# Optimization experiments

Measured on AMD Instinct MI355X. Metric: run time of the kernel, lower is better.

The kernel has to match this reference:

```python
import jax, jax.numpy as jnp
import numpy as np

C = 768           # input_embed_dim
G = 16            # conv groups
CG = C // G       # channels per group (48)
MAX_TOKENS = 64
N = 65536         # sequence / spatial length
B = 1             # .item() in the torch code forces batch == 1
EPS = 1e-5


def _layernorm(x, gamma, beta):
    mu = jnp.mean(x, axis=-1, keepdims=True)
    var = jnp.mean((x - mu) ** 2, axis=-1, keepdims=True)
    return (x - mu) * jax.lax.rsqrt(var + EPS) * gamma + beta


def _grouped_pointwise(x, w):
    # x: [B, N, C]; w: [G, CG_out, CG_in] (torch Conv2d weight [C, CG, 1, 1] regrouped)
    xg = x.reshape(x.shape[0], x.shape[1], G, CG)           # [B, N, G, CG]
    yg = jnp.einsum('bngi,goi->bngo', xg, w)                 # [B, N, G, CG]
    return yg.reshape(x.shape[0], x.shape[1], C)


def setup_inputs() -> dict:
    key = jax.random.key(0)
    ks = jax.random.split(key, 9)
    s = 1.0 / np.sqrt(CG)
    inp = {
        'x': jax.random.normal(ks[0], (B, N, C), dtype=jnp.float32),
        'tn_gamma': jnp.ones((C,), jnp.float32),
        'tn_beta': jnp.zeros((C,), jnp.float32),
        'w1': jax.random.uniform(ks[1], (G, CG, CG), jnp.float32, -s, s),   # grouped conv 1
        'w2': jax.random.uniform(ks[2], (MAX_TOKENS, C), jnp.float32, -1 / np.sqrt(C), 1 / np.sqrt(C)),  # pointwise conv C->MAX_TOKENS
        'wf': jax.random.uniform(ks[3], (G, CG, CG), jnp.float32, -s, s),   # grouped feat conv
        'pred_w': jax.random.uniform(ks[4], (C,), jnp.float32, -1 / np.sqrt(C), 1 / np.sqrt(C)),
        'pred_b': jax.random.uniform(ks[5], (1,), jnp.float32, -1 / np.sqrt(C), 1 / np.sqrt(C)),
        'n_gamma': jnp.ones((C,), jnp.float32),
        'n_beta': jnp.zeros((C,), jnp.float32),
    }
    return inp


def reference(x, tn_gamma, tn_beta, w1, w2, wf, pred_w, pred_b, n_gamma, n_beta):
    # LayerNorm over channels
    xn = _layernorm(x, tn_gamma, tn_beta)                    # [B, N, C]

    # token_predictor: AdaptiveAvgPool2d over (N,1) -> Linear(C,1) -> Sigmoid
    pooled = jnp.mean(xn, axis=1)                            # [B, C]
    ratio = jax.nn.sigmoid(pooled @ pred_w + pred_b[0])      # [B]
    # num_tokens = int(ratio.item() * MAX_TOKENS)  (truncation == floor, ratio > 0)
    num_tokens = jnp.floor(ratio[0] * MAX_TOKENS).astype(jnp.int32)
    tok_mask = (jnp.arange(MAX_TOKENS) < num_tokens)[None, :, None]  # [1, T, 1]

    # tokenLearner: grouped 1x1 conv -> ReLU -> pointwise conv C -> MAX_TOKENS
    h = jax.nn.relu(_grouped_pointwise(xn, w1))              # [B, N, C]
    scores = jnp.einsum('bnc,tc->btn', h, w2)                # [B, T, N]
    # softmax is per-token-row over N, so slicing rows before/after softmax is equivalent;
    # we mask dropped rows to zero (fixed output shape instead of dynamic slice).
    selected = jax.nn.softmax(scores, axis=-1)
    selected = jnp.where(tok_mask, selected, 0.0)            # [B, T, N]

    feat = _grouped_pointwise(xn, wf)                        # [B, N, C]
    out = jnp.einsum('btn,bnc->btc', selected, feat)         # [B, T, C]
    out = _layernorm(out, n_gamma, n_beta)
    out = jnp.where(tok_mask, out, 0.0)                      # zero rows beyond num_tokens
    return selected, out
```

## Files before the change

kernel.cpp:

```cpp
#include <hip/hip_runtime.h>
#include <hip/hip_bf16.h>

#define DEV __device__ __forceinline__

constexpr int N = 65536;
constexpr int C = 768;
constexpr int T = 64;

using bf16 = __hip_bfloat16;
using short8 = __attribute__((ext_vector_type(8))) short;
using f32x4  = __attribute__((ext_vector_type(4))) float;

DEV ushort f2bits(float v) { union { __hip_bfloat16 h; ushort u; } x; x.h = __float2bfloat16(v); return x.u; }
DEV float bits2f(ushort b) { union { uint u; float f; } x; x.u = ((uint)b) << 16; return x.f; }
DEV f32x4 mfma16(short8 a, short8 b, f32x4 c) { return __builtin_amdgcn_mfma_f32_16x16x32_bf16(a, b, c, 0, 0, 0); }
DEV int swz(int row, int col) { return row * 64 + (col ^ ((row & 7) << 3)); }

DEV float wredsum(float v) {
#pragma unroll
  for (int o = 32; o > 0; o >>= 1) v += __shfl_xor(v, o, 64);
  return v;
}

__global__ __launch_bounds__(256) void k_wprep(const float* __restrict__ w1,
                                               const float* __restrict__ w2,
                                               const float* __restrict__ wf,
                                               short* __restrict__ w1p,
                                               short* __restrict__ w2p,
                                               short* __restrict__ wfp) {
  const int b = blockIdx.x, tid = threadIdx.x;
  if (b < 192) {
    int idx = b * 256 + tid;
    int j = idx & 7, lane = (idx >> 3) & 63, u = idx >> 9;
    int kt = u & 1, v = u >> 1, ot = v % 3, g = v / 3;
    int o = ot * 16 + (lane & 15), k = kt * 32 + ((lane >> 4) & 3) * 8 + j;
    w1p[idx] = (k < 48) ? (short)f2bits(w1[g * 2304 + o * 48 + k]) : (short)0;
  } else if (b < 448) {
    int idx = (b - 192) * 256 + tid;
    int j = idx & 7, lane = (idx >> 3) & 63, u = idx >> 9;
    int kt = u & 1, v = u >> 1, tt = v & 3, g = v >> 2;
    int t = tt * 16 + (lane & 15), k = kt * 32 + ((lane >> 4) & 3) * 8 + j;
    w2p[idx] = (k < 48) ? (short)f2bits(w2[t * 768 + g * 48 + k]) : (short)0;
  } else {
    int idx = (b - 448) * 256 + tid;
    int j = idx & 7, lane = (idx >> 3) & 63, u = idx >> 9;
    int kt = u & 1, v = u >> 1, ot = v % 3, g = v / 3;
    int o = ot * 16 + (lane & 15), k = kt * 32 + ((lane >> 4) & 3) * 8 + j;
    wfp[idx] = (k < 48) ? (short)f2bits(wf[g * 2304 + o * 48 + k]) : (short)0;
  }
}

__global__ __launch_bounds__(256, 4) void k_ln(const float4* __restrict__ x,
                                               const float4* __restrict__ gam,
                                               const float4* __restrict__ bet,
                                               uint2* __restrict__ xn,
                                               float* __restrict__ pooled) {
  const int tid = threadIdx.x, wave = tid >> 6, lane = tid & 63;
  float4 gg[3], bb[3], pool[3];
#pragma unroll
  for (int j = 0; j < 3; j++) {
    gg[j] = gam[lane + 64 * j]; bb[j] = bet[lane + 64 * j];
    pool[j] = make_float4(0.f, 0.f, 0.f, 0.f);
  }
  const int r0 = (blockIdx.x * 4 + wave) * 16;
  for (int r = r0; r < r0 + 16; ++r) {
    const float4* xr = x + (size_t)r * 192;
    float4 v[3]; float s = 0.f, q = 0.f;
#pragma unroll
    for (int j = 0; j < 3; j++) {
      v[j] = xr[lane + 64 * j];
      s += v[j].x + v[j].y + v[j].z + v[j].w;
      q += v[j].x * v[j].x + v[j].y * v[j].y + v[j].z * v[j].z + v[j].w * v[j].w;
    }
    s = wredsum(s); q = wredsum(q);
    const float mu = s * (1.f / C);
    const float rs = rsqrtf(q * (1.f / C) - mu * mu + 1e-5f);
    uint2* xo = xn + (size_t)r * 192;
#pragma unroll
    for (int j = 0; j < 3; j++) {
      float y0 = (v[j].x - mu) * rs * gg[j].x + bb[j].x;
      float y1 = (v[j].y - mu) * rs * gg[j].y + bb[j].y;
      float y2 = (v[j].z - mu) * rs * gg[j].z + bb[j].z;
      float y3 = (v[j].w - mu) * rs * gg[j].w + bb[j].w;
      pool[j].x += y0; pool[j].y += y1; pool[j].z += y2; pool[j].w += y3;
      xo[lane + 64 * j] = make_uint2((uint)f2bits(y0) | ((uint)f2bits(y1) << 16),
                                     (uint)f2bits(y2) | ((uint)f2bits(y3) << 16));
    }
  }
  __shared__ float lp[4][C];
#pragma unroll
  for (int j = 0; j < 3; j++) {
    int base = (lane + 64 * j) * 4;
    lp[wave][base] = pool[j].x; lp[wave][base + 1] = pool[j].y;
    lp[wave][base + 2] = pool[j].z; lp[wave][base + 3] = pool[j].w;
  }
  __syncthreads();
  for (int c = tid; c < C; c += 256)
    atomicAdd(&pooled[c], lp[0][c] + lp[1][c] + lp[2][c] + lp[3][c]);
}

__global__ __launch_bounds__(256) void k_pool(const float* __restrict__ pooled,
                                              const float* __restrict__ pw,
                                              const float* __restrict__ pb,
                                              int* __restrict__ ntok) {
  const int tid = threadIdx.x, wave = tid >> 6, lane = tid & 63;
  float a = 0.f;
  for (int c = tid; c < C; c += 256) a += pooled[c] * (1.f / N) * pw[c];
  a = wredsum(a);
  __shared__ float red[4];
  if (lane == 0) red[wave] = a;
  __syncthreads();
  if (tid == 0) {
    float d = red[0] + red[1] + red[2] + red[3] + pb[0];
    float ratio = 1.f / (1.f + expf(-d));
    int nt = (int)floorf(ratio * 64.f);
    nt = nt < 0 ? 0 : (nt > 64 ? 64 : nt);
    *ntok = nt;
  }
}

__global__ __launch_bounds__(256, 4) void k_cs(const short* __restrict__ xn,
                                               const short* __restrict__ w1p,
                                               const short* __restrict__ w2p,
                                               float* __restrict__ scores) {
  __shared__ __align__(16) short hs[4][16 * 64];
  const int tid = threadIdx.x, wave = tid >> 6, lane = tid & 63;
  const int l15 = lane & 15, g2 = lane >> 4;
  short* hw = hs[wave];
  {
    uint* hz = (uint*)hw;
    for (int i = lane; i < 512; i += 64) hz[i] = 0u;
  }
  const int row0 = blockIdx.x * 64 + wave * 16;
  f32x4 acc[4];
#pragma unroll
  for (int t = 0; t < 4; ++t) acc[t] = (f32x4){0.f, 0.f, 0.f, 0.f};
  const short* xrow = xn + (size_t)(row0 + l15) * 768;
  const int lo8 = lane * 8;

  short8 bx0 = *(const short8*)(xrow + g2 * 8);
  short8 bx1 = *(const short8*)(xrow + 32 + g2 * 8);
  for (int g = 0; g < 16; ++g) {
    const int gn = (g < 15) ? g + 1 : 15;
    short8 nbx0 = *(const short8*)(xrow + gn * 48 + g2 * 8);
    short8 nbx1 = *(const short8*)(xrow + gn * 48 + 32 + g2 * 8);
    const short* w1g = w1p + g * 3072;
#pragma unroll
    for (int ot = 0; ot < 3; ++ot) {
      short8 a0 = *(const short8*)(w1g + (ot * 2 + 0) * 512 + lo8);
      short8 a1 = *(const short8*)(w1g + (ot * 2 + 1) * 512 + lo8);
      f32x4 h = (f32x4){0.f, 0.f, 0.f, 0.f};
      h = mfma16(a0, bx0, h);
      h = mfma16(a1, bx1, h);
      uint lo = (uint)f2bits(fmaxf(h[0], 0.f)) | ((uint)f2bits(fmaxf(h[1], 0.f)) << 16);
      uint hi = (uint)f2bits(fmaxf(h[2], 0.f)) | ((uint)f2bits(fmaxf(h[3], 0.f)) << 16);
      *(uint2*)&hw[swz(l15, ot * 16 + g2 * 4)] = make_uint2(lo, hi);
    }
    short8 hb0 = *(const short8*)&hw[swz(l15, g2 * 8)];
    short8 hb1 = *(const short8*)&hw[swz(l15, 32 + g2 * 8)];
    const short* w2g = w2p + g * 4096;
#pragma unroll
    for (int tt = 0; tt < 4; ++tt) {
      short8 a0 = *(const short8*)(w2g + (tt * 2 + 0) * 512 + lo8);
      short8 a1 = *(const short8*)(w2g + (tt * 2 + 1) * 512 + lo8);
      acc[tt] = mfma16(a0, hb0, acc[tt]);
      acc[tt] = mfma16(a1, hb1, acc[tt]);
    }
    bx0 = nbx0; bx1 = nbx1;
  }
#pragma unroll
  for (int tt = 0; tt < 4; ++tt)
#pragma unroll
    for (int r = 0; r < 4; ++r)
      scores[(size_t)(tt * 16 + g2 * 4 + r) * N + row0 + l15] = acc[tt][r];
}

__global__ __launch_bounds__(256) void k_stats(const float* __restrict__ scores,
                                               float2* __restrict__ part) {
  const int t = blockIdx.x >> 3, s = blockIdx.x & 7;
  const float* row = scores + (size_t)t * N + s * 8192;
  float m = -1e30f, l = 0.f;
  for (int i = threadIdx.x; i < 8192; i += 256) {
    float v = row[i];
    if (v > m) { l = l * __expf(m - v) + 1.f; m = v; }
    else       { l += __expf(v - m); }
  }
#pragma unroll
  for (int o = 32; o > 0; o >>= 1) {
    float m2 = __shfl_xor(m, o, 64), l2 = __shfl_xor(l, o, 64);
    float M = fmaxf(m, m2);
    l = l * __expf(m - M) + l2 * __expf(m2 - M); m = M;
  }
  __shared__ float sm[4], sl[4];
  const int wave = threadIdx.x >> 6, lane = threadIdx.x & 63;
  if (lane == 0) { sm[wave] = m; sl[wave] = l; }
  __syncthreads();
  if (threadIdx.x == 0) {
    float M = sm[0], L = sl[0];
    for (int w = 1; w < 4; w++) { float M2 = fmaxf(M, sm[w]); L = L * __expf(M - M2) + sl[w] * __expf(sm[w] - M2); M = M2; }
    part[blockIdx.x] = make_float2(M, L);
  }
}

__global__ void k_sfinal(const float2* __restrict__ part, float* __restrict__ Mv,
                         float* __restrict__ Li) {
  int t = threadIdx.x;
  float M = -1e30f, L = 0.f;
  for (int s = 0; s < 8; s++) {
    float2 p = part[t * 8 + s];
    float M2 = fmaxf(M, p.x);
    L = L * __expf(M - M2) + p.y * __expf(p.x - M2); M = M2;
  }
  Mv[t] = M; Li[t] = 1.f / L;
}

__global__ __launch_bounds__(256) void k_sel(const float* __restrict__ scores,
                                             const float* __restrict__ Mv,
                                             const float* __restrict__ Li,
                                             const int* __restrict__ ntokp,
                                             float* __restrict__ sel) {
  const int t = blockIdx.x >> 3, s = blockIdx.x & 7;
  const size_t base = (size_t)t * N + s * 8192;
  const bool on = t < *ntokp;
  const float m = Mv[t], li = Li[t];
  for (int i = threadIdx.x; i < 8192; i += 256)
    sel[base + i] = on ? __expf(scores[base + i] - m) * li : 0.f;
}

__global__ __launch_bounds__(512, 4) void k_og(const short* __restrict__ xn,
                                               const short* __restrict__ wfp,
                                               const float* __restrict__ sel,
                                               const int* __restrict__ ntokp,
                                               ushort* __restrict__ out_part) {
  __shared__ __align__(16) short ft[192 * 64];
  const int tid = threadIdx.x, wave = tid >> 6, lane = tid & 63;
  const int l15 = lane & 15, g2 = lane >> 4;
  const int cb = blockIdx.y, nb = blockIdx.x;
  const int ntok = *ntokp;
  const int tt = wave >> 1, chalf = wave & 1;
  const int gq = wave >> 1, ntq = wave & 1;
  const bool act = (tt * 16) < ntok;
  short8 wa0[3], wa1[3];
  {
    const short* wb = wfp + (size_t)(cb * 4 + gq) * 3072 + lane * 8;
#pragma unroll
    for (int ot = 0; ot < 3; ++ot) {
      wa0[ot] = *(const short8*)(wb + (ot * 2 + 0) * 512);
      wa1[ot] = *(const short8*)(wb + (ot * 2 + 1) * 512);
    }
  }
  f32x4 acc[6];
#pragma unroll
  for (int k = 0; k < 6; ++k) acc[k] = (f32x4){0.f, 0.f, 0.f, 0.f};

  for (int ns = 0; ns < 16; ++ns) {
    const int n0 = nb * 512 + ns * 32;
    __syncthreads();
    {
      const short* xr = xn + (size_t)(n0 + ntq * 16 + l15) * 768 + (cb * 4 + gq) * 48;
      short8 b0 = *(const short8*)(xr + g2 * 8);
      short8 b1 = *(const short8*)(xr + 32 + g2 * 8);
#pragma unroll
      for (int ot = 0; ot < 3; ++ot) {
        f32x4 d = (f32x4){0.f, 0.f, 0.f, 0.f};
        d = mfma16(wa0[ot], b0, d);
        d = mfma16(wa1[ot], b1, d);
        int n = ntq * 16 + l15;
#pragma unroll
        for (int r = 0; r < 4; ++r) {
          int c = gq * 48 + ot * 16 + g2 * 4 + r;
          ft[c * 64 + (n ^ ((c & 7) << 3))] = (short)f2bits(d[r]);
        }
      }
    }
    __syncthreads();
    if (act) {
      const float* sr = sel + (size_t)(tt * 16 + l15) * N + n0 + g2 * 8;
      float4 s0 = *(const float4*)sr;
      float4 s1 = *(const float4*)(sr + 4);
      short8 pa;
      pa[0] = (short)f2bits(s0.x); pa[1] = (short)f2bits(s0.y);
      pa[2] = (short)f2bits(s0.z); pa[3] = (short)f2bits(s0.w);
      pa[4] = (short)f2bits(s1.x); pa[5] = (short)f2bits(s1.y);
      pa[6] = (short)f2bits(s1.z); pa[7] = (short)f2bits(s1.w);
#pragma unroll
      for (int ct = 0; ct < 6; ++ct) {
        int c = (chalf * 6 + ct) * 16 + l15;
        short8 fb = *(const short8*)&ft[c * 64 + ((g2 * 8) ^ ((c & 7) << 3))];
        acc[ct] = mfma16(pa, fb, acc[ct]);
      }
    }
  }
#pragma unroll
  for (int ct = 0; ct < 6; ++ct)
#pragma unroll
    for (int r = 0; r < 4; ++r) {
      int t = tt * 16 + g2 * 4 + r;
      int c = cb * 192 + (chalf * 6 + ct) * 16 + l15;
      out_part[(size_t)nb * (64 * 768) + t * 768 + c] = f2bits(acc[ct][r]);
    }
}

__global__ __launch_bounds__(256) void k_red(const ushort* __restrict__ out_part,
                                             float* __restrict__ oacc) {
  int i = blockIdx.x * 256 + threadIdx.x;
  float s = 0.f;
  for (int nb = 0; nb < 128; ++nb) s += bits2f(out_part[(size_t)nb * (64 * 768) + i]);
  oacc[i] = s;
}

__global__ __launch_bounds__(256) void k_ofinal(const float* __restrict__ out_acc,
                                                const float* __restrict__ ng,
                                                const float* __restrict__ nb_,
                                                const int* __restrict__ ntokp,
                                                float* __restrict__ outp) {
  const int tid = threadIdx.x, wave = tid >> 6, lane = tid & 63;
  const int ntok = *ntokp;
  for (int t = wave; t < T; t += 4) {
    const float* r = out_acc + t * C;
    float v[12]; float s = 0.f;
#pragma unroll
    for (int j = 0; j < 12; j++) { v[j] = r[lane + 64 * j]; s += v[j]; }
    s = wredsum(s); float mu = s * (1.f / C);
    float q = 0.f;
#pragma unroll
    for (int j = 0; j < 12; j++) { float d = v[j] - mu; q += d * d; }
    q = wredsum(q); float rs = rsqrtf(q * (1.f / C) + 1e-5f);
    float* o = outp + t * C;
#pragma unroll
    for (int j = 0; j < 12; j++) {
      int c = lane + 64 * j;
      float y = (v[j] - mu) * rs * ng[c] + nb_[c];
      o[c] = (t < ntok) ? y : 0.f;
    }
  }
}

extern "C" void kernel_launch(void* const* d_in, const int* in_sizes, int n_in,
                              void* d_out, int out_size, void* d_ws, size_t ws_size,
                              hipStream_t stream) {
  const float* x  = (const float*)d_in[0];
  const float* tg = (const float*)d_in[1];
  const float* tb = (const float*)d_in[2];
  const float* w1 = (const float*)d_in[3];
  const float* w2 = (const float*)d_in[4];
  const float* wf = (const float*)d_in[5];
  const float* pw = (const float*)d_in[6];
  const float* pb = (const float*)d_in[7];
  const float* ng = (const float*)d_in[8];
  const float* nb = (const float*)d_in[9];

  char* ws = (char*)d_ws;
  float*  pooled = (float*)(ws + 0);
  float2* part   = (float2*)(ws + 4096);
  float*  Mv     = (float*)(ws + 8192);
  float*  Li     = (float*)(ws + 8448);
  int*    ntok   = (int*)(ws + 8704);
  short*  w1p    = (short*)(ws + 16384);
  short*  w2p    = (short*)(ws + 114688);
  short*  wfp    = (short*)(ws + 245760);
  short*  xn     = (short*)(ws + 344064);
  float*  scores = (float*)(ws + 101007360);
  ushort* opart  = (ushort*)(ws + 101007360);
  float*  oacc   = (float*)(ws + 113590272);

  float* sel  = (float*)d_out;
  float* outp = (float*)d_out + (size_t)T * N;

  hipMemsetAsync(pooled, 0, C * sizeof(float), stream);

  k_wprep <<<640, 256, 0, stream>>>(w1, w2, wf, w1p, w2p, wfp);
  k_ln    <<<1024, 256, 0, stream>>>((const float4*)x, (const float4*)tg, (const float4*)tb,
                                     (uint2*)xn, pooled);
  k_pool  <<<1, 256, 0, stream>>>(pooled, pw, pb, ntok);
  k_cs    <<<1024, 256, 0, stream>>>(xn, w1p, w2p, scores);
  k_stats <<<512, 256, 0, stream>>>(scores, part);
  k_sfinal<<<1, 64, 0, stream>>>(part, Mv, Li);
  k_sel   <<<512, 256, 0, stream>>>(scores, Mv, Li, ntok, sel);
  k_og    <<<dim3(128, 4), 512, 0, stream>>>(xn, wfp, sel, ntok, opart);
  k_red   <<<192, 256, 0, stream>>>(opart, oacc);
  k_ofinal<<<1, 256, 0, stream>>>(oacc, ng, nb, ntok, outp);
}
```

Measured before the change: 465.4 us.

## Double-buffer LDS in score and output kernels, fuse softmax finalisation and reductions

Several changes land together. k_cs gets a double-buffered per-wave h tile and a 2x unroll. k_sfinal is merged into k_sel, which now vectorises with float4 and also writes a bf16 copy of the selection matrix. k_og reads that bf16 copy instead of converting fp32, double-buffers its LDS feature tile with register prefetch of the next x and selection loads, cuts to one barrier per step, and packs LDS stores. k_red and k_ofinal are fused into one 64-block k_fin. The goal is fewer launches, less traffic and less barrier stalling, at the cost of extra LDS (which lowers k_og occupancy to 2), an extra bf16 write, and a one-pass variance that is less numerically robust.

Result: faster. 438.4 us (-5.8%).

```diff
diff --git a/kernel.cpp b/kernel.cpp
--- a/kernel.cpp
+++ b/kernel.cpp
@@ -123,13 +123,12 @@
                                                const short* __restrict__ w1p,
                                                const short* __restrict__ w2p,
                                                float* __restrict__ scores) {
-  __shared__ __align__(16) short hs[4][16 * 64];
+  __shared__ __align__(16) short hs[4][2][16 * 64];
   const int tid = threadIdx.x, wave = tid >> 6, lane = tid & 63;
   const int l15 = lane & 15, g2 = lane >> 4;
-  short* hw = hs[wave];
   {
-    uint* hz = (uint*)hw;
-    for (int i = lane; i < 512; i += 64) hz[i] = 0u;
+    uint* hz = (uint*)hs[wave];
+    for (int i = lane; i < 1024; i += 64) hz[i] = 0u;
   }
   const int row0 = blockIdx.x * 64 + wave * 16;
   f32x4 acc[4];
@@ -140,10 +139,12 @@
 
   short8 bx0 = *(const short8*)(xrow + g2 * 8);
   short8 bx1 = *(const short8*)(xrow + 32 + g2 * 8);
+#pragma unroll 2
   for (int g = 0; g < 16; ++g) {
     const int gn = (g < 15) ? g + 1 : 15;
     short8 nbx0 = *(const short8*)(xrow + gn * 48 + g2 * 8);
     short8 nbx1 = *(const short8*)(xrow + gn * 48 + 32 + g2 * 8);
+    short* hw = hs[wave][g & 1];
     const short* w1g = w1p + g * 3072;
 #pragma unroll
     for (int ot = 0; ot < 3; ++ot) {
@@ -202,94 +203,103 @@
   }
 }
 
-__global__ void k_sfinal(const float2* __restrict__ part, float* __restrict__ Mv,
-                         float* __restrict__ Li) {
-  int t = threadIdx.x;
+__global__ __launch_bounds__(256) void k_sel(const float* __restrict__ scores,
+                                             const float2* __restrict__ part,
+                                             const int* __restrict__ ntokp,
+                                             float* __restrict__ sel,
+                                             ushort* __restrict__ selb) {
+  const int t = blockIdx.x >> 3, s = blockIdx.x & 7;
   float M = -1e30f, L = 0.f;
-  for (int s = 0; s < 8; s++) {
-    float2 p = part[t * 8 + s];
+#pragma unroll
+  for (int i = 0; i < 8; i++) {
+    float2 p = part[t * 8 + i];
     float M2 = fmaxf(M, p.x);
     L = L * __expf(M - M2) + p.y * __expf(p.x - M2); M = M2;
   }
-  Mv[t] = M; Li[t] = 1.f / L;
-}
-
-__global__ __launch_bounds__(256) void k_sel(const float* __restrict__ scores,
-                                             const float* __restrict__ Mv,
-                                             const float* __restrict__ Li,
-                                             const int* __restrict__ ntokp,
-                                             float* __restrict__ sel) {
-  const int t = blockIdx.x >> 3, s = blockIdx.x & 7;
+  const float li = 1.f / L;
+  const bool on = t < *ntokp;
   const size_t base = (size_t)t * N + s * 8192;
-  const bool on = t < *ntokp;
-  const float m = Mv[t], li = Li[t];
-  for (int i = threadIdx.x; i < 8192; i += 256)
-    sel[base + i] = on ? __expf(scores[base + i] - m) * li : 0.f;
-}
-
-__global__ __launch_bounds__(512, 4) void k_og(const short* __restrict__ xn,
+  const float4* sp = (const float4*)(scores + base);
+  float4* op = (float4*)(sel + base);
+  uint2* ob = (uint2*)(selb + base);
+#pragma unroll
+  for (int it = 0; it < 8; ++it) {
+    int idx = threadIdx.x + 256 * it;
+    float4 v = sp[idx];
+    float4 e;
+    e.x = on ? __expf(v.x - M) * li : 0.f;
+    e.y = on ? __expf(v.y - M) * li : 0.f;
+    e.z = on ? __expf(v.z - M) * li : 0.f;
+    e.w = on ? __expf(v.w - M) * li : 0.f;
+    op[idx] = e;
+    ob[idx] = make_uint2((uint)f2bits(e.x) | ((uint)f2bits(e.y) << 16),
+                         (uint)f2bits(e.z) | ((uint)f2bits(e.w) << 16));
+  }
+}
+
+__global__ __launch_bounds__(512, 2) void k_og(const short* __restrict__ xn,
                                                const short* __restrict__ wfp,
-                                               const float* __restrict__ sel,
+                                               const short* __restrict__ selb,
                                                const int* __restrict__ ntokp,
                                                ushort* __restrict__ out_part) {
-  __shared__ __align__(16) short ft[192 * 64];
+  __shared__ __align__(16) short ft[2][192 * 64];
   const int tid = threadIdx.x, wave = tid >> 6, lane = tid & 63;
   const int l15 = lane & 15, g2 = lane >> 4;
   const int cb = blockIdx.y, nb = blockIdx.x;
   const int ntok = *ntokp;
+  const int gq = wave >> 1, ntq = wave & 1;
   const int tt = wave >> 1, chalf = wave & 1;
-  const int gq = wave >> 1, ntq = wave & 1;
   const bool act = (tt * 16) < ntok;
-  short8 wa0[3], wa1[3];
+  short8 wb0[3], wb1[3];
   {
     const short* wb = wfp + (size_t)(cb * 4 + gq) * 3072 + lane * 8;
 #pragma unroll
     for (int ot = 0; ot < 3; ++ot) {
-      wa0[ot] = *(const short8*)(wb + (ot * 2 + 0) * 512);
-      wa1[ot] = *(const short8*)(wb + (ot * 2 + 1) * 512);
+      wb0[ot] = *(const short8*)(wb + (ot * 2 + 0) * 512);
+      wb1[ot] = *(const short8*)(wb + (ot * 2 + 1) * 512);
     }
   }
   f32x4 acc[6];
 #pragma unroll
   for (int k = 0; k < 6; ++k) acc[k] = (f32x4){0.f, 0.f, 0.f, 0.f};
 
-  for (int ns = 0; ns < 16; ++ns) {
-    const int n0 = nb * 512 + ns * 32;
-    __syncthreads();
-    {
-      const short* xr = xn + (size_t)(n0 + ntq * 16 + l15) * 768 + (cb * 4 + gq) * 48;
-      short8 b0 = *(const short8*)(xr + g2 * 8);
-      short8 b1 = *(const short8*)(xr + 32 + g2 * 8);
+  const short* xr0 = xn + (size_t)(nb * 512 + ntq * 16 + l15) * 768 + (cb * 4 + gq) * 48;
+  const short* sr0 = selb + (size_t)(tt * 16 + l15) * N + nb * 512 + g2 * 8;
+
+  short8 bx0 = *(const short8*)(xr0 + g2 * 8);
+  short8 bx1 = *(const short8*)(xr0 + 32 + g2 * 8);
+  short8 ps = {};
+  short8 nx0 = bx0, nx1 = bx1, nps = ps;
+
+  for (int ns = 0; ns <= 16; ++ns) {
+    if (ns < 16) {
+      const int nsn = (ns < 15) ? ns + 1 : 15;
+      nx0 = *(const short8*)(xr0 + nsn * 24576 + g2 * 8);
+      nx1 = *(const short8*)(xr0 + nsn * 24576 + 32 + g2 * 8);
+      nps = *(const short8*)(sr0 + ns * 32);
+      short* f = ft[ns & 1];
 #pragma unroll
       for (int ot = 0; ot < 3; ++ot) {
         f32x4 d = (f32x4){0.f, 0.f, 0.f, 0.f};
-        d = mfma16(wa0[ot], b0, d);
-        d = mfma16(wa1[ot], b1, d);
-        int n = ntq * 16 + l15;
-#pragma unroll
-        for (int r = 0; r < 4; ++r) {
-          int c = gq * 48 + ot * 16 + g2 * 4 + r;
-          ft[c * 64 + (n ^ ((c & 7) << 3))] = (short)f2bits(d[r]);
-        }
+        d = mfma16(bx0, wb0[ot], d);
+        d = mfma16(bx1, wb1[ot], d);
+        int c = gq * 48 + ot * 16 + l15;
+        uint lo = (uint)f2bits(d[0]) | ((uint)f2bits(d[1]) << 16);
+        uint hi = (uint)f2bits(d[2]) | ((uint)f2bits(d[3]) << 16);
+        *(uint2*)&f[c * 64 + ((ntq * 16 + g2 * 4) ^ ((c & 7) << 3))] = make_uint2(lo, hi);
       }
     }
-    __syncthreads();
-    if (act) {
-      const float* sr = sel + (size_t)(tt * 16 + l15) * N + n0 + g2 * 8;
-      float4 s0 = *(const float4*)sr;
-      float4 s1 = *(const float4*)(sr + 4);
-      short8 pa;
-      pa[0] = (short)f2bits(s0.x); pa[1] = (short)f2bits(s0.y);
-      pa[2] = (short)f2bits(s0.z); pa[3] = (short)f2bits(s0.w);
-      pa[4] = (short)f2bits(s1.x); pa[5] = (short)f2bits(s1.y);
-      pa[6] = (short)f2bits(s1.z); pa[7] = (short)f2bits(s1.w);
+    if (ns >= 1 && act) {
+      const short* f = ft[(ns - 1) & 1];
 #pragma unroll
       for (int ct = 0; ct < 6; ++ct) {
         int c = (chalf * 6 + ct) * 16 + l15;
-        short8 fb = *(const short8*)&ft[c * 64 + ((g2 * 8) ^ ((c & 7) << 3))];
-        acc[ct] = mfma16(pa, fb, acc[ct]);
+        short8 fb = *(const short8*)&f[c * 64 + ((g2 * 8) ^ ((c & 7) << 3))];
+        acc[ct] = mfma16(ps, fb, acc[ct]);
       }
     }
+    __syncthreads();
+    bx0 = nx0; bx1 = nx1; ps = nps;
   }
 #pragma unroll
   for (int ct = 0; ct < 6; ++ct)
@@ -301,39 +311,38 @@
     }
 }
 
-__global__ __launch_bounds__(256) void k_red(const ushort* __restrict__ out_part,
-                                             float* __restrict__ oacc) {
-  int i = blockIdx.x * 256 + threadIdx.x;
-  float s = 0.f;
-  for (int nb = 0; nb < 128; ++nb) s += bits2f(out_part[(size_t)nb * (64 * 768) + i]);
-  oacc[i] = s;
-}
-
-__global__ __launch_bounds__(256) void k_ofinal(const float* __restrict__ out_acc,
-                                                const float* __restrict__ ng,
-                                                const float* __restrict__ nb_,
-                                                const int* __restrict__ ntokp,
-                                                float* __restrict__ outp) {
-  const int tid = threadIdx.x, wave = tid >> 6, lane = tid & 63;
-  const int ntok = *ntokp;
-  for (int t = wave; t < T; t += 4) {
-    const float* r = out_acc + t * C;
-    float v[12]; float s = 0.f;
-#pragma unroll
-    for (int j = 0; j < 12; j++) { v[j] = r[lane + 64 * j]; s += v[j]; }
-    s = wredsum(s); float mu = s * (1.f / C);
-    float q = 0.f;
-#pragma unroll
-    for (int j = 0; j < 12; j++) { float d = v[j] - mu; q += d * d; }
-    q = wredsum(q); float rs = rsqrtf(q * (1.f / C) + 1e-5f);
-    float* o = outp + t * C;
-#pragma unroll
-    for (int j = 0; j < 12; j++) {
-      int c = lane + 64 * j;
-      float y = (v[j] - mu) * rs * ng[c] + nb_[c];
-      o[c] = (t < ntok) ? y : 0.f;
-    }
-  }
+__global__ __launch_bounds__(192) void k_fin(const ushort* __restrict__ out_part,
+                                             const float* __restrict__ ng,
+                                             const float* __restrict__ nb_,
+                                             const int* __restrict__ ntokp,
+                                             float* __restrict__ outp) {
+  const int t = blockIdx.x, tid = threadIdx.x;
+  const int wave = tid >> 6, lane = tid & 63;
+  const int c4 = tid * 4;
+  float4 s = make_float4(0.f, 0.f, 0.f, 0.f);
+  const ushort* base = out_part + t * 768 + c4;
+  for (int nbk = 0; nbk < 128; ++nbk) {
+    uint2 v = *(const uint2*)(base + (size_t)nbk * 49152);
+    s.x += bits2f((ushort)(v.x & 0xffff)); s.y += bits2f((ushort)(v.x >> 16));
+    s.z += bits2f((ushort)(v.y & 0xffff)); s.w += bits2f((ushort)(v.y >> 16));
+  }
+  float ss = s.x + s.y + s.z + s.w;
+  float qq = s.x * s.x + s.y * s.y + s.z * s.z + s.w * s.w;
+  ss = wredsum(ss); qq = wredsum(qq);
+  __shared__ float sm[3], sq[3];
+  if (lane == 0) { sm[wave] = ss; sq[wave] = qq; }
+  __syncthreads();
+  const float S = sm[0] + sm[1] + sm[2], Q = sq[0] + sq[1] + sq[2];
+  const float mu = S * (1.f / C);
+  const float rs = rsqrtf(Q * (1.f / C) - mu * mu + 1e-5f);
+  const bool on = t < *ntokp;
+  float4 g = *(const float4*)(ng + c4), b = *(const float4*)(nb_ + c4);
+  float4 y;
+  y.x = on ? (s.x - mu) * rs * g.x + b.x : 0.f;
+  y.y = on ? (s.y - mu) * rs * g.y + b.y : 0.f;
+  y.z = on ? (s.z - mu) * rs * g.z + b.z : 0.f;
+  y.w = on ? (s.w - mu) * rs * g.w + b.w : 0.f;
+  *(float4*)(outp + t * 768 + c4) = y;
 }
 
 extern "C" void kernel_launch(void* const* d_in, const int* in_sizes, int n_in,
@@ -353,8 +362,6 @@
   char* ws = (char*)d_ws;
   float*  pooled = (float*)(ws + 0);
   float2* part   = (float2*)(ws + 4096);
-  float*  Mv     = (float*)(ws + 8192);
-  float*  Li     = (float*)(ws + 8448);
   int*    ntok   = (int*)(ws + 8704);
   short*  w1p    = (short*)(ws + 16384);
   short*  w2p    = (short*)(ws + 114688);
@@ -362,12 +369,12 @@
   short*  xn     = (short*)(ws + 344064);
   float*  scores = (float*)(ws + 101007360);
   ushort* opart  = (ushort*)(ws + 101007360);
-  float*  oacc   = (float*)(ws + 113590272);
+  ushort* selb   = (ushort*)(ws + 117784576);
 
   float* sel  = (float*)d_out;
   float* outp = (float*)d_out + (size_t)T * N;
 
-  hipMemsetAsync(pooled, 0, C * sizeof(float), stream);
+  (void)hipMemsetAsync(pooled, 0, C * sizeof(float), stream);
 
   k_wprep <<<640, 256, 0, stream>>>(w1, w2, wf, w1p, w2p, wfp);
   k_ln    <<<1024, 256, 0, stream>>>((const float4*)x, (const float4*)tg, (const float4*)tb,
@@ -375,9 +382,7 @@
   k_pool  <<<1, 256, 0, stream>>>(pooled, pw, pb, ntok);
   k_cs    <<<1024, 256, 0, stream>>>(xn, w1p, w2p, scores);
   k_stats <<<512, 256, 0, stream>>>(scores, part);
-  k_sfinal<<<1, 64, 0, stream>>>(part, Mv, Li);
-  k_sel   <<<512, 256, 0, stream>>>(scores, Mv, Li, ntok, sel);
-  k_og    <<<dim3(128, 4), 512, 0, stream>>>(xn, wfp, sel, ntok, opart);
-  k_red   <<<192, 256, 0, stream>>>(opart, oacc);
-  k_ofinal<<<1, 256, 0, stream>>>(oacc, ng, nb, ntok, outp);
-}
+  k_sel   <<<512, 256, 0, stream>>>(scores, part, ntok, sel, selb);
+  k_og    <<<dim3(128, 4), 512, 0, stream>>>(xn, wfp, (const short*)selb, ntok, opart);
+  k_fin   <<<64, 192, 0, stream>>>(opart, ng, nb, ntok, outp);
+}
```
